# Kernel tuning notes

Hardware: AMD Instinct MI355X
Metric: run time of the kernel (lower is better)

The kernel has to match this reference:

```python
import jax, jax.numpy as jnp
import numpy as np

B, T, F, D, H, DFF, L = 8, 1024, 64, 512, 8, 2048, 3
DH = D // H
PERIODS = np.array([16, 256, 4096], np.int32)
CMS_LRS = np.array([0.01, 0.001, 0.0001], np.float32)
TITANS_LR = 0.01
TITANS_CLIP = 0.1


def layernorm(x, w, b):
    m = x.mean(-1, keepdims=True)
    v = x.var(-1, keepdims=True)
    return (x - m) * jax.lax.rsqrt(v + 1e-5) * w + b


def setup_inputs() -> dict:
    key = jax.random.key(0)
    ks = jax.random.split(key, 40)
    f32 = jnp.float32
    def rn(i, shape, s=0.02):
        return jax.random.normal(ks[i], shape, f32) * s
    inp = {
        'x': jax.random.normal(ks[0], (B, T, F), f32),
        'titans_W': jnp.zeros((D, D), f32),
        'cms_summary': jnp.zeros((L, D), f32),
        'cms_buf_sum': jnp.zeros((L, D), f32),
        'cms_count': jnp.zeros((L,), jnp.int32),
        'cms_step': jnp.zeros((L,), jnp.int32),
        'in_norm_w': jnp.ones((F,), f32), 'in_norm_b': jnp.zeros((F,), f32),
        'in_proj_W': rn(1, (D, F)), 'in_proj_b': jnp.zeros((D,), f32),
        'W_base': rn(2, (D, D), 0.01),
        'tit_out_W': rn(3, (D, D)), 'tit_out_b': jnp.zeros((D,), f32),
        'gate_W': rn(4, (L, D, D)), 'gate_b': jnp.zeros((L, D), f32),
        'comb_W': rn(5, (D, L * D)), 'comb_b': jnp.zeros((D,), f32),
        'n1_w': jnp.ones((D,), f32), 'n1_b': jnp.zeros((D,), f32),
        'qkv_W': rn(6, (3 * D, D)), 'qkv_b': jnp.zeros((3 * D,), f32),
        'ao_W': rn(7, (D, D)), 'ao_b': jnp.zeros((D,), f32),
        'n2_w': jnp.ones((D,), f32), 'n2_b': jnp.zeros((D,), f32),
        'f1_W': rn(8, (DFF, D)), 'f1_b': jnp.zeros((DFF,), f32),
        'f2_W': rn(9, (D, DFF)), 'f2_b': jnp.zeros((D,), f32),
        'fn_w': jnp.ones((D,), f32), 'fn_b': jnp.zeros((D,), f32),
        'head_W': rn(10, (1, D)), 'head_b': jnp.zeros((1,), f32),
    }
    return inp


def cms_tick_all(means, summary, buf_sum, count, step, gate_W, gate_b):
    """Sequential tick over T timesteps, vectorized over the L levels.
    means: [T, D] batch-mean of final hidden at each timestep."""
    periods = jnp.asarray(PERIODS)
    lrs = jnp.asarray(CMS_LRS)
    def step_fn(carry, m):
        summ, bs, cnt, stp = carry
        bs = bs + m[None, :]              # [L, D]
        cnt = cnt + 1
        stp = stp + 1
        fire = cnt >= periods              # [L]
        acc = bs / cnt.astype(bs.dtype)[:, None]
        g = jax.nn.sigmoid(jnp.einsum('lij,lj->li', gate_W, acc) + gate_b)
        new_summ = jnp.where(fire[:, None], (1.0 - lrs)[:, None] * summ + lrs[:, None] * g * acc, summ)
        bs = jnp.where(fire[:, None], jnp.zeros_like(bs), bs)
        cnt = jnp.where(fire, jnp.zeros_like(cnt), cnt)
        return (new_summ, bs, cnt, stp), None
    (summary, buf_sum, count, step), _ = jax.lax.scan(step_fn, (summary, buf_sum, count, step), means)
    return summary, buf_sum, count, step


def reference(x, titans_W, cms_summary, cms_buf_sum, cms_count, cms_step,
              in_norm_w, in_norm_b, in_proj_W, in_proj_b,
              W_base, tit_out_W, tit_out_b,
              gate_W, gate_b, comb_W, comb_b,
              n1_w, n1_b, qkv_W, qkv_b, ao_W, ao_b,
              n2_w, n2_b, f1_W, f1_b, f2_W, f2_b,
              fn_w, fn_b, head_W, head_b):
    # input norm + projection: [B,T,F] -> [B,T,D]
    h = layernorm(x, in_norm_w, in_norm_b) @ in_proj_W.T + in_proj_b
    # Titans fast-weight read
    W = W_base + titans_W
    tit = (h @ W.T) @ tit_out_W.T + tit_out_b
    # Titans fast-weight update (detached in the original)
    hs = jax.lax.stop_gradient(h)
    target = hs.mean(axis=1)               # [B, D]
    query = hs[:, -1, :]                   # [B, D]
    pred_m = query @ titans_W.T
    err = (target - pred_m).mean(axis=0)   # [D]
    grad = jnp.outer(err, query.mean(axis=0))
    gn = jnp.linalg.norm(grad)
    grad = jnp.where(gn > TITANS_CLIP, grad * (TITANS_CLIP / gn), grad)
    new_W = titans_W + TITANS_LR * grad
    h = h + tit
    # CMS residual from current summaries: concat [L*D] -> combine -> [D]
    cms_out = cms_summary.reshape(L * D) @ comb_W.T + comb_b
    h = h + cms_out                        # broadcast over [B,T,D]
    # transformer block (pre-norm, causal MHA)
    hn = layernorm(h, n1_w, n1_b)
    qkv = hn @ qkv_W.T + qkv_b
    q, k, v = jnp.split(qkv, 3, axis=-1)
    def to_heads(t):
        return t.reshape(B, T, H, DH).transpose(0, 2, 1, 3)
    q, k, v = to_heads(q), to_heads(k), to_heads(v)
    scores = jnp.einsum('bhqd,bhkd->bhqk', q, k) / np.sqrt(DH).astype(np.float32)
    causal = jnp.triu(jnp.ones((T, T), bool), 1)
    scores = jnp.where(causal, -jnp.inf, scores)
    attn = jax.nn.softmax(scores, axis=-1)
    ao = jnp.einsum('bhqk,bhkd->bhqd', attn, v).transpose(0, 2, 1, 3).reshape(B, T, D)
    h = h + ao @ ao_W.T + ao_b
    hn2 = layernorm(h, n2_w, n2_b)
    h = h + jax.nn.gelu(hn2 @ f1_W.T + f1_b, approximate=False) @ f2_W.T + f2_b
    h = layernorm(h, fn_w, fn_b)
    pred = (h @ head_W.T + head_b).squeeze(-1)   # [B, T]
    # CMS tick over all T steps (detached in the original)
    means = jax.lax.stop_gradient(h).mean(axis=0)  # [T, D]
    ns, nb, nc, nt = cms_tick_all(means, cms_summary, cms_buf_sum, cms_count, cms_step, gate_W, gate_b)
    return pred, new_W, ns, nb, nc, nt
```

## Files before the change

kernel.cpp:

```cpp
#include <hip/hip_runtime.h>
#include <hip/hip_bf16.h>
#include <math.h>

#define Bdim 8
#define Tdim 1024
#define Fdim 64
#define Ddim 512
#define Lcms 3

#define OFF_PRED 0
#define OFF_W    8192
#define OFF_NS   270336
#define OFF_NB   271872
#define OFF_NC   273408
#define OFF_NT   273411

typedef __hip_bfloat16 bf16;
typedef __attribute__((ext_vector_type(8))) short s8;
typedef __attribute__((ext_vector_type(4))) float f4;

__device__ __forceinline__ float b2f(bf16 v){ return __bfloat162float(v); }
__device__ __forceinline__ bf16  f2b(float v){ return __float2bfloat16(v); }
__device__ __forceinline__ short fb16(float v){ bf16 t = __float2bfloat16(v); return *reinterpret_cast<short*>(&t); }
__device__ __forceinline__ float toF(float v){ return v; }
__device__ __forceinline__ float toF(bf16 v){ return __bfloat162float(v); }
template<typename T> __device__ __forceinline__ T fromF(float v);
template<> __device__ __forceinline__ float fromF<float>(float v){ return v; }
template<> __device__ __forceinline__ bf16  fromF<bf16 >(float v){ return f2b(v); }

__device__ __forceinline__ f4 mfma16(s8 a, s8 b, f4 c){
  return __builtin_amdgcn_mfma_f32_16x16x32_bf16(a, b, c, 0, 0, 0);
}

__device__ __forceinline__ void gload16(const bf16* g, bf16* l){
  __builtin_amdgcn_global_load_lds(
      (const __attribute__((address_space(1))) unsigned*)g,
      (__attribute__((address_space(3))) unsigned*)l, 16, 0, 0);
}

__device__ __forceinline__ float gelu_fast(float x){
  float z2 = 1.5957691216f*(x + 0.044715f*x*x*x);
  z2 = fminf(fmaxf(z2, -18.f), 18.f);
  return x / (1.f + __expf(-z2));
}

__global__ __launch_bounds__(256) void k_conv_all(
    const void* s0, const void* s1, const void* s2, const void* s3,
    const void* s4, const void* s5, const void* s6, const void* s7,
    const void* s8v, const void* s9, const void* s10, const void* s11,
    const void* s12, const void* s13,
    bf16* __restrict__ dst, const unsigned* __restrict__ w1, int* __restrict__ flag,
    const int* __restrict__ cnt, int* __restrict__ params){
  bool isbf = (w1[0] == 0x3F803F80u);
  if (blockIdx.x==0 && threadIdx.x==0){
    flag[0] = isbf ? 1 : 0;
    const int P[3] = {16,256,4096};
    for (int l=0;l<3;l++){
      int c0 = cnt[l];
      int t1 = P[l] - c0 - 1; if (t1 < 0) t1 = 0;
      int K = (t1 >= Tdim) ? 0 : 1 + (Tdim-1-t1)/P[l];
      params[l*4+0]=t1; params[l*4+1]=K; params[l*4+2]=c0+t1+1; params[l*4+3]=c0;
    }
  }
  const void* srcs[14] = {s0,s1,s2,s3,s4,s5,s6,s7,s8v,s9,s10,s11,s12,s13};
  const int   ns[14]   = {262144,512,786432,1536,262144,512,1048576,2048,1048576,512,
                          32768,512,786432,1536};
  int gstride = gridDim.x*blockDim.x;
  int gid = blockIdx.x*blockDim.x + threadIdx.x;
  int base = 0;
  #pragma unroll
  for (int s=0;s<14;s++){
    int n = ns[s];
    if (isbf){
      const short* sp = (const short*)srcs[s]; short* dp = (short*)(dst+base);
      for (int i=gid;i<n;i+=gstride) dp[i] = sp[i];
    } else {
      const float* sp = (const float*)srcs[s];
      for (int i=gid;i<n;i+=gstride) dst[base+i] = f2b(sp[i]);
    }
    base += n;
  }
}

template<typename TW>
__device__ __forceinline__ void lnx_impl(const TW* x, const TW* nw, const TW* nb_, bf16* xn){
  int row = blockIdx.x*4 + (threadIdx.x>>6);
  int lane = threadIdx.x & 63;
  float v = toF(x[(size_t)row*Fdim + lane]);
  float s = v, s2 = v*v;
  #pragma unroll
  for (int off=32; off; off>>=1){ s += __shfl_down(s,off); s2 += __shfl_down(s2,off); }
  s = __shfl(s, 0); s2 = __shfl(s2, 0);
  float mu = s*(1.f/64.f);
  float var = s2*(1.f/64.f) - mu*mu;
  float rstd = rsqrtf(var + 1e-5f);
  xn[(size_t)row*Fdim + lane] = f2b((v-mu)*rstd*toF(nw[lane]) + toF(nb_[lane]));
}
__global__ __launch_bounds__(256) void k_lnx(const void* x, const void* nw, const void* nb_,
    bf16* xn, const int* flg){
  if (*flg) lnx_impl<bf16>((const bf16*)x,(const bf16*)nw,(const bf16*)nb_,xn);
  else      lnx_impl<float>((const float*)x,(const float*)nw,(const float*)nb_,xn);
}

__global__ __launch_bounds__(256) void k_reduce_tq1(const bf16* __restrict__ h,
    float* __restrict__ redtmp){
  int b = blockIdx.x>>5, chunk = blockIdx.x&31;
  int tid = threadIdx.x;
  #pragma unroll
  for (int o=0;o<2;o++){
    int d = tid + o*256;
    const bf16* p = h + ((size_t)b*Tdim + chunk*32)*Ddim + d;
    float s = 0.f;
    #pragma unroll
    for (int t=0;t<32;t++) s += b2f(p[(size_t)t*Ddim]);
    redtmp[((size_t)b*32 + chunk)*Ddim + d] = s;
  }
}

template<typename TW>
__device__ __forceinline__ void misc1_impl(const TW* Wbse, const TW* tW, bf16* Wout,
    const TW* summ, const TW* combW, const TW* combb, float* outv,
    const bf16* h, const float* redtmp, float* target, float* query){
  int blk = blockIdx.x, tid = threadIdx.x;
  if (blk < 1024){
    int i = blk*256 + tid;
    Wout[i] = f2b(toF(Wbse[i]) + toF(tW[i]));
  } else if (blk < 1152){
    __shared__ float s_s[Lcms*Ddim];
    for (int i=tid;i<Lcms*Ddim;i+=256) s_s[i] = toF(summ[i]);
    __syncthreads();
    int wave = tid>>6, lane = tid&63;
    int d = (blk-1024)*4 + wave;
    const TW* wr = combW + (size_t)d*(Lcms*Ddim);
    float a = 0.f;
    for (int j=lane;j<Lcms*Ddim;j+=64) a += s_s[j]*toF(wr[j]);
    #pragma unroll
    for (int off=32; off; off>>=1) a += __shfl_down(a,off);
    if (lane==0) outv[d] = a + toF(combb[d]);
  } else {
    int i = (blk-1152)*256 + tid;
    int b = i>>9, d = i&511;
    float s = 0.f;
    #pragma unroll
    for (int c=0;c<32;c++) s += redtmp[((size_t)b*32+c)*Ddim + d];
    target[i] = s*(1.f/(float)Tdim);
    query[i]  = b2f(h[((size_t)b*Tdim + (Tdim-1))*Ddim + d]);
  }
}
__global__ __launch_bounds__(256) void k_misc1(const void* Wbse, const void* tW, bf16* Wout,
    const void* summ, const void* combW, const void* combb, float* outv,
    const bf16* h, const float* redtmp, float* target, float* query, const int* flg){
  if (*flg) misc1_impl<bf16>((const bf16*)Wbse,(const bf16*)tW,Wout,(const bf16*)summ,
                             (const bf16*)combW,(const bf16*)combb,outv,h,redtmp,target,query);
  else      misc1_impl<float>((const float*)Wbse,(const float*)tW,Wout,(const float*)summ,
                             (const float*)combW,(const float*)combb,outv,h,redtmp,target,query);
}

template<typename TW>
__device__ __forceinline__ void titans_err_impl(const float* target, const float* query,
    const TW* tW, float* err, float* qmean){
  int wave = threadIdx.x>>6, lane = threadIdx.x&63;
  int d = blockIdx.x*4 + wave;
  const TW* wr = tW + (size_t)d*Ddim;
  float s = 0.f;
  #pragma unroll
  for (int b=0;b<Bdim;b++){
    const float* q = query + b*Ddim;
    float p = 0.f;
    for (int j=lane;j<Ddim;j+=64) p += q[j]*toF(wr[j]);
    s += p;
  }
  #pragma unroll
  for (int off=32; off; off>>=1) s += __shfl_down(s,off);
  if (lane==0){
    float e=0.f, qm=0.f;
    #pragma unroll
    for (int b=0;b<Bdim;b++){ e += target[b*Ddim+d]; qm += query[b*Ddim+d]; }
    err[d]   = (e - s)*(1.f/(float)Bdim);
    qmean[d] = qm*(1.f/(float)Bdim);
  }
}
__global__ __launch_bounds__(256) void k_titans_err(const float* target, const float* query,
    const void* tW, float* err, float* qmean, const int* flg){
  if (*flg) titans_err_impl<bf16>(target,query,(const bf16*)tW,err,qmean);
  else      titans_err_impl<float>(target,query,(const float*)tW,err,qmean);
}

template<typename TW>
__device__ __forceinline__ void new_W_impl(const TW* tW, const float* err, const float* qmean,
    TW* outW){
  int tid = threadIdx.x;
  float a = err[tid]*err[tid] + err[tid+256]*err[tid+256];
  float b = qmean[tid]*qmean[tid] + qmean[tid+256]*qmean[tid+256];
  #pragma unroll
  for (int off=32; off; off>>=1){ a += __shfl_down(a,off); b += __shfl_down(b,off); }
  __shared__ float sa[4], sb[4];
  int lane = tid & 63, wid = tid >> 6;
  if (lane==0){ sa[wid]=a; sb[wid]=b; }
  __syncthreads();
  float A = sa[0]+sa[1]+sa[2]+sa[3];
  float Bq= sb[0]+sb[1]+sb[2]+sb[3];
  float gn = sqrtf(A*Bq);
  float sf = 0.01f * (gn > 0.1f ? 0.1f/gn : 1.0f);
  int i = blockIdx.x*256 + tid;
  int r = i >> 9, c = i & 511;
  outW[i] = fromF<TW>(toF(tW[i]) + sf*err[r]*qmean[c]);
}
__global__ __launch_bounds__(256) void k_new_W(const void* tW, const float* err,
    const float* qmean, void* out, const int* flg){
  if (*flg) new_W_impl<bf16>((const bf16*)tW, err, qmean, ((bf16*)out)+OFF_W);
  else      new_W_impl<float>((const float*)tW, err, qmean, ((float*)out)+OFF_W);
}

template<int MODE, int DEPTH>
__global__ __launch_bounds__(512) void gemm_mfma(const bf16* __restrict__ A,
    const bf16* __restrict__ Bw, const bf16* __restrict__ bias,
    const float* __restrict__ colvec, bf16* __restrict__ Cout,
    const bf16* __restrict__ resid, int M, int N, int K){
  __shared__ __align__(16) bf16 As[DEPTH][128*32];
  __shared__ __align__(16) bf16 Bs[DEPTH][128*32];
  int tid = threadIdx.x, wave = tid>>6, lane = tid&63, quad = lane>>4, l16 = lane&15;
  int row0 = blockIdx.x*128, col0 = blockIdx.y*128;
  int wr = (wave>>2)*64, wc = (wave&3)*32;
  int srow = wave*16 + (lane>>2);
  int scol = (((lane&3) ^ ((lane>>3)&3)))*8;
  int rswz = (quad ^ ((l16>>1)&3))*8;
  f4 acc[8] = {};
  int niter = K >> 5;
  #define STAGE(bu, k0) { \
    gload16(A  + (size_t)(row0 + srow)*K + (k0) + scol, &As[bu][wave*512 + lane*8]); \
    gload16(Bw + (size_t)(col0 + srow)*K + (k0) + scol, &Bs[bu][wave*512 + lane*8]); \
  }
  STAGE(0, 0)
  if (DEPTH >= 3 && niter > 1) STAGE(1, 32)
  if (DEPTH >= 4 && niter > 2) STAGE(2, 64)
  for (int k=0; k<niter; k++){
    int bu = k & (DEPTH-1);
    if (DEPTH == 2){
      if (k+1 < niter){
        STAGE((k+1)&1, (k+1)<<5)
        asm volatile("s_waitcnt vmcnt(2)" ::: "memory");
      } else {
        asm volatile("s_waitcnt vmcnt(0)" ::: "memory");
      }
    } else {
      if (k+3 < niter){
        STAGE((k+3)&3, (k+3)<<5)
        asm volatile("s_waitcnt vmcnt(6)" ::: "memory");
      } else if (k+2 < niter){
        asm volatile("s_waitcnt vmcnt(4)" ::: "memory");
      } else if (k+1 < niter){
        asm volatile("s_waitcnt vmcnt(2)" ::: "memory");
      } else {
        asm volatile("s_waitcnt vmcnt(0)" ::: "memory");
      }
    }
    __builtin_amdgcn_s_barrier();
    s8 af[4], bfv[2];
    #pragma unroll
    for (int i=0;i<4;i++) af[i]  = *reinterpret_cast<const s8*>(&As[bu][(wr + i*16 + l16)*32 + rswz]);
    #pragma unroll
    for (int j=0;j<2;j++) bfv[j] = *reinterpret_cast<const s8*>(&Bs[bu][(wc + j*16 + l16)*32 + rswz]);
    #pragma unroll
    for (int i=0;i<4;i++)
      #pragma unroll
      for (int j=0;j<2;j++)
        acc[i*2+j] = mfma16(af[i], bfv[j], acc[i*2+j]);
    asm volatile("s_waitcnt lgkmcnt(0)" ::: "memory");
    __builtin_amdgcn_s_barrier();
  }
  #undef STAGE
  #pragma unroll
  for (int i=0;i<4;i++){
    #pragma unroll
    for (int j=0;j<2;j++){
      int n = col0 + wc + j*16 + l16;
      f4 a = acc[i*2+j];
      #pragma unroll
      for (int r=0;r<4;r++){
        int m = row0 + wr + i*16 + quad*4 + r;
        float v = a[r];
        if (MODE & 1) v += b2f(bias[n]);
        if (MODE & 8) v += colvec[n];
        if (MODE & 4) v = gelu_fast(v);
        if (MODE & 2) v += b2f(resid[(size_t)m*Ddim + n]);
        Cout[(size_t)m*N + n] = f2b(v);
      }
    }
  }
}

template<typename TW, int HEAD>
__device__ __forceinline__ void ln_impl(const bf16* in, const TW* w, const TW* b, bf16* outp,
    const TW* hw, const TW* hb, TW* pred){
  int row = blockIdx.x;
  const bf16* r = in + (size_t)row*Ddim;
  int tid = threadIdx.x;
  float v0 = b2f(r[tid]), v1 = b2f(r[tid + 256]);
  float s = v0+v1, s2 = v0*v0 + v1*v1;
  #pragma unroll
  for (int off=32; off; off>>=1){ s += __shfl_down(s,off); s2 += __shfl_down(s2,off); }
  __shared__ float sa[4], sb[4], sc[4];
  int lane = tid & 63, wid = tid >> 6;
  if (lane==0){ sa[wid]=s; sb[wid]=s2; }
  __syncthreads();
  float ts  = sa[0]+sa[1]+sa[2]+sa[3];
  float ts2 = sb[0]+sb[1]+sb[2]+sb[3];
  float mu = ts*(1.f/(float)Ddim);
  float var = ts2*(1.f/(float)Ddim) - mu*mu;
  float rstd = rsqrtf(var + 1e-5f);
  float o0 = (v0-mu)*rstd*toF(w[tid])     + toF(b[tid]);
  float o1 = (v1-mu)*rstd*toF(w[tid+256]) + toF(b[tid+256]);
  outp[(size_t)row*Ddim + tid]       = f2b(o0);
  outp[(size_t)row*Ddim + tid + 256] = f2b(o1);
  if (HEAD){
    float sp = o0*toF(hw[tid]) + o1*toF(hw[tid+256]);
    #pragma unroll
    for (int off=32; off; off>>=1) sp += __shfl_down(sp,off);
    if (lane==0) sc[wid] = sp;
    __syncthreads();
    if (tid==0) pred[row] = fromF<TW>(sc[0]+sc[1]+sc[2]+sc[3] + toF(hb[0]));
  }
}
template<int HEAD>
__global__ __launch_bounds__(256) void k_ln(const bf16* in, const void* w, const void* b,
    bf16* outp, const void* hw, const void* hb, void* out, const int* flg){
  if (*flg) ln_impl<bf16,HEAD>(in,(const bf16*)w,(const bf16*)b,outp,
                               (const bf16*)hw,(const bf16*)hb,((bf16*)out)+OFF_PRED);
  else      ln_impl<float,HEAD>(in,(const float*)w,(const float*)b,outp,
                               (const float*)hw,(const float*)hb,((float*)out)+OFF_PRED);
}

__global__ __launch_bounds__(256) void k_attn_mfma(const bf16* __restrict__ qkv,
                                                   bf16* __restrict__ ao){
  int blk = blockIdx.x;
  int bh = blk & 63;
  int qt = 15 - (blk >> 6);
  int head = bh & 7, b = bh >> 3;
  __shared__ __align__(16) bf16 Ks[2][64][72];
  __shared__ __align__(16) unsigned Vt4[2][64*36];
  __shared__ __align__(16) bf16 Ps[4][16][72];
  int tid = threadIdx.x, wave = tid>>6, lane = tid&63, quad = lane>>4, l16 = lane&15;
  int q0w = qt*64 + wave*16;
  const bf16* basep = qkv + (size_t)b*Tdim*1536 + head*64;
  s8 qf0 = *reinterpret_cast<const s8*>(basep + (size_t)(q0w+l16)*1536 + quad*8);
  s8 qf1 = *reinterpret_cast<const s8*>(basep + (size_t)(q0w+l16)*1536 + 32 + quad*8);
  f4 o[4] = {{0,0,0,0},{0,0,0,0},{0,0,0,0},{0,0,0,0}};
  float m_r[4] = {-3.0e38f,-3.0e38f,-3.0e38f,-3.0e38f};
  float l_r[4] = {0.f,0.f,0.f,0.f};
  int key_s = tid>>3, dgk = (tid&7)*8;
  int vp = tid>>3, dgv = (tid&7)*8;
  int vu4 = (((vp>>2) ^ (tid&7)) & 7)*4 + (vp&3);
  int nch = qt + 1;
  s8 kr0[2], kr1[2], vra[2], vrb[2];
  {
    const bf16* kp = basep + (size_t)key_s*1536 + 512 + dgk;
    kr0[0] = *reinterpret_cast<const s8*>(kp);
    kr1[0] = *reinterpret_cast<const s8*>(kp + (size_t)32*1536);
    const bf16* vpa = basep + (size_t)(2*vp)*1536 + 1024 + dgv;
    vra[0] = *reinterpret_cast<const s8*>(vpa);
    vrb[0] = *reinterpret_cast<const s8*>(vpa + 1536);
    if (1 < nch){
      const bf16* kp1 = basep + (size_t)(64+key_s)*1536 + 512 + dgk;
      kr0[1] = *reinterpret_cast<const s8*>(kp1);
      kr1[1] = *reinterpret_cast<const s8*>(kp1 + (size_t)32*1536);
      const bf16* vpa1 = basep + (size_t)(64 + 2*vp)*1536 + 1024 + dgv;
      vra[1] = *reinterpret_cast<const s8*>(vpa1);
      vrb[1] = *reinterpret_cast<const s8*>(vpa1 + 1536);
    }
  }
  auto do_chunk = [&](int ch, int bu){
    f4 sc4[4] = {{0,0,0,0},{0,0,0,0},{0,0,0,0},{0,0,0,0}};
    #pragma unroll
    for (int t=0;t<4;t++){
      sc4[t] = mfma16(qf0, *reinterpret_cast<const s8*>(&Ks[bu][t*16+l16][quad*8]),    sc4[t]);
      sc4[t] = mfma16(qf1, *reinterpret_cast<const s8*>(&Ks[bu][t*16+l16][32+quad*8]), sc4[t]);
    }
    int key0 = ch*64 + l16;
    #pragma unroll
    for (int r=0;r<4;r++){
      int qrow = q0w + quad*4 + r;
      float a0 = (key0      <= qrow) ? sc4[0][r]*0.125f : -3.0e38f;
      float a1 = (key0 + 16 <= qrow) ? sc4[1][r]*0.125f : -3.0e38f;
      float a2 = (key0 + 32 <= qrow) ? sc4[2][r]*0.125f : -3.0e38f;
      float a3 = (key0 + 48 <= qrow) ? sc4[3][r]*0.125f : -3.0e38f;
      float mx = fmaxf(fmaxf(a0,a1), fmaxf(a2,a3));
      mx = fmaxf(mx, __shfl_xor(mx,1)); mx = fmaxf(mx, __shfl_xor(mx,2));
      mx = fmaxf(mx, __shfl_xor(mx,4)); mx = fmaxf(mx, __shfl_xor(mx,8));
      float mnew = fmaxf(m_r[r], mx);
      float al = __expf(m_r[r]-mnew); m_r[r] = mnew;
      float p0 = __expf(a0-mnew), p1 = __expf(a1-mnew);
      float p2 = __expf(a2-mnew), p3 = __expf(a3-mnew);
      float rs = (p0+p1)+(p2+p3);
      rs += __shfl_xor(rs,1); rs += __shfl_xor(rs,2);
      rs += __shfl_xor(rs,4); rs += __shfl_xor(rs,8);
      l_r[r] = l_r[r]*al + rs;
      o[0][r]*=al; o[1][r]*=al; o[2][r]*=al; o[3][r]*=al;
      int prow = quad*4+r;
      *reinterpret_cast<short*>(&Ps[wave][prow][l16])    = fb16(p0);
      *reinterpret_cast<short*>(&Ps[wave][prow][16+l16]) = fb16(p1);
      *reinterpret_cast<short*>(&Ps[wave][prow][32+l16]) = fb16(p2);
      *reinterpret_cast<short*>(&Ps[wave][prow][48+l16]) = fb16(p3);
    }
    asm volatile("s_waitcnt lgkmcnt(0)" ::: "memory");
    s8 pf0 = *reinterpret_cast<const s8*>(&Ps[wave][l16][quad*8]);
    s8 pf1 = *reinterpret_cast<const s8*>(&Ps[wave][l16][32+quad*8]);
    #pragma unroll
    for (int j=0;j<4;j++){
      int d = j*16 + l16;
      int swz = (d>>3) & 7;
      s8 b0 = *reinterpret_cast<const s8*>(&Vt4[bu][d*36 + ((quad   ^ swz))*4]);
      s8 b1 = *reinterpret_cast<const s8*>(&Vt4[bu][d*36 + (((4+quad)^ swz))*4]);
      o[j] = mfma16(pf0, b0, o[j]);
      o[j] = mfma16(pf1, b1, o[j]);
    }
  };
  for (int ch0=0; ch0<nch; ch0+=2){
    #pragma unroll
    for (int s=0;s<2;s++){
      if (ch0+s < nch){
        *reinterpret_cast<s8*>(&Ks[s][key_s][dgk])    = kr0[s];
        *reinterpret_cast<s8*>(&Ks[s][32+key_s][dgk]) = kr1[s];
        #pragma unroll
        for (int j=0;j<8;j++){
          unsigned w = (unsigned)(unsigned short)vra[s][j] | ((unsigned)(unsigned short)vrb[s][j] << 16);
          Vt4[s][(dgv+j)*36 + vu4] = w;
        }
      }
    }
    __syncthreads();
    #pragma unroll
    for (int s=0;s<2;s++){
      int chn = ch0 + 2 + s;
      if (chn < nch){
        const bf16* kp = basep + (size_t)(chn*64+key_s)*1536 + 512 + dgk;
        kr0[s] = *reinterpret_cast<const s8*>(kp);
        kr1[s] = *reinterpret_cast<const s8*>(kp + (size_t)32*1536);
        const bf16* vpa = basep + (size_t)(chn*64 + 2*vp)*1536 + 1024 + dgv;
        vra[s] = *reinterpret_cast<const s8*>(vpa);
        vrb[s] = *reinterpret_cast<const s8*>(vpa + 1536);
      }
    }
    do_chunk(ch0, 0);
    if (ch0+1 < nch) do_chunk(ch0+1, 1);
    if (ch0+2 < nch) __syncthreads();
  }
  #pragma unroll
  for (int r=0;r<4;r++){
    float inv = 1.f/l_r[r];
    size_t rowb = (size_t)(b*Tdim + q0w + quad*4 + r)*Ddim + head*64;
    ao[rowb + l16]      = f2b(o[0][r]*inv);
    ao[rowb + 16 + l16] = f2b(o[1][r]*inv);
    ao[rowb + 32 + l16] = f2b(o[2][r]*inv);
    ao[rowb + 48 + l16] = f2b(o[3][r]*inv);
  }
}

__global__ void k_means(const bf16* __restrict__ h, float* __restrict__ means){
  int i = blockIdx.x*256 + threadIdx.x;
  float s = 0.f;
  #pragma unroll
  for (int b=0;b<Bdim;b++) s += b2f(h[(size_t)b*Tdim*Ddim + i]);
  means[i] = s*(1.f/(float)Bdim);
}

template<typename TW>
__device__ __forceinline__ void cms_acc_impl(const float* means, const TW* bs0,
    const int* params, float* acc, bf16* acch, float* tailtmp){
  int tid = threadIdx.x;
  if (blockIdx.x < 384){
    int l = blockIdx.x>>7, k = blockIdx.x&127;
    int K = params[l*4+1];
    if (k >= K){
      for (int d=tid; d<Ddim; d+=256) acch[((size_t)l*128+k)*Ddim + d] = f2b(0.f);
      return;
    }
    int t1 = params[l*4], cnt0 = params[l*4+2];
    const int P[3] = {16,256,4096};
    int lo = (k==0) ? 0 : t1 + (k-1)*P[l] + 1;
    int hi = t1 + k*P[l];
    float inv = 1.f/((k==0) ? (float)cnt0 : (float)P[l]);
    int lane = tid&63, strip = tid>>6;
    __shared__ float red[4][Ddim];
    float4 a0 = {0,0,0,0}, a1 = {0,0,0,0};
    for (int t=lo+strip; t<=hi; t+=4){
      const float4* row = (const float4*)(means + (size_t)t*Ddim);
      float4 v0 = row[lane], v1 = row[lane+64];
      a0.x+=v0.x; a0.y+=v0.y; a0.z+=v0.z; a0.w+=v0.w;
      a1.x+=v1.x; a1.y+=v1.y; a1.z+=v1.z; a1.w+=v1.w;
    }
    ((float4*)red[strip])[lane]    = a0;
    ((float4*)red[strip])[lane+64] = a1;
    __syncthreads();
    for (int d=tid; d<Ddim; d+=256){
      float s = red[0][d]+red[1][d]+red[2][d]+red[3][d];
      if (k==0) s += toF(bs0[l*Ddim+d]);
      float v = s*inv;
      acc[((size_t)l*65+k)*Ddim + d] = v;
      acch[((size_t)l*128+k)*Ddim + d] = f2b(v);
    }
  } else {
    int bb = blockIdx.x - 384;
    int l = bb>>5, chunk = bb&31;
    int t1 = params[l*4], K = params[l*4+1];
    const int P[3] = {16,256,4096};
    int lo = (K==0) ? 0 : t1 + (K-1)*P[l] + 1;
    int f = tid & 127, strip = tid >> 7;
    int tbeg = chunk*32, tend = tbeg + 32;
    if (tbeg < lo) tbeg = lo;
    float4 a = {0,0,0,0};
    for (int t=tbeg+strip; t<tend; t+=2){
      float4 v = ((const float4*)(means + (size_t)t*Ddim))[f];
      a.x+=v.x; a.y+=v.y; a.z+=v.z; a.w+=v.w;
    }
    __shared__ float4 redt[2][128];
    redt[strip][f] = a;
    __syncthreads();
    if (strip==0){
      float4 b = redt[1][f];
      a.x+=b.x; a.y+=b.y; a.z+=b.z; a.w+=b.w;
      ((float4*)(tailtmp + ((size_t)l*32 + chunk)*Ddim))[f] = a;
    }
  }
}
__global__ __launch_bounds__(256) void k_cms_acc(const float* means, const void* bs0,
    const int* params, float* acc, bf16* acch, float* tailtmp, const int* flg){
  if (*flg) cms_acc_impl<bf16>(means,(const bf16*)bs0,params,acc,acch,tailtmp);
  else      cms_acc_impl<float>(means,(const float*)bs0,params,acc,acch,tailtmp);
}

__global__ __launch_bounds__(256) void k_cms_gate_mfma(const bf16* __restrict__ accbh,
    const bf16* __restrict__ wg, const bf16* __restrict__ wgb, float* __restrict__ g){
  int l = blockIdx.y;
  const bf16* A  = accbh + (size_t)l*128*Ddim;
  const bf16* Bw = wg    + (size_t)l*Ddim*Ddim;
  __shared__ __align__(16) bf16 As[128*32];
  __shared__ __align__(16) bf16 Bs[128*32];
  int tid = threadIdx.x, wave = tid>>6, lane = tid&63, quad = lane>>4, l16 = lane&15;
  int col0 = blockIdx.x*128;
  int wr = (wave>>1)*64, wc = (wave&1)*64;
  int srow = lane>>2, scol = (lane&3)*8;
  f4 acc[16] = {};
  for (int k0=0; k0<Ddim; k0+=32){
    __syncthreads();
    #pragma unroll
    for (int it=0; it<2; it++){
      int c = wave*2 + it;
      gload16(A  + (size_t)(c*16 + srow)*Ddim + k0 + scol, &As[c*512 + lane*8]);
      gload16(Bw + (size_t)(col0 + c*16 + srow)*Ddim + k0 + scol, &Bs[c*512 + lane*8]);
    }
    __syncthreads();
    s8 af[4], bfv[4];
    #pragma unroll
    for (int i=0;i<4;i++) af[i]  = *reinterpret_cast<const s8*>(&As[(wr + i*16 + l16)*32 + quad*8]);
    #pragma unroll
    for (int j=0;j<4;j++) bfv[j] = *reinterpret_cast<const s8*>(&Bs[(wc + j*16 + l16)*32 + quad*8]);
    #pragma unroll
    for (int i=0;i<4;i++)
      #pragma unroll
      for (int j=0;j<4;j++)
        acc[i*4+j] = mfma16(af[i], bfv[j], acc[i*4+j]);
  }
  #pragma unroll
  for (int i=0;i<4;i++){
    #pragma unroll
    for (int j=0;j<4;j++){
      int n = col0 + wc + j*16 + l16;
      f4 a = acc[i*4+j];
      #pragma unroll
      for (int r=0;r<4;r++){
        int m = wr + i*16 + quad*4 + r;
        if (m < 65){
          float v = a[r] + b2f(wgb[l*Ddim + n]);
          g[((size_t)l*65 + m)*Ddim + n] = 1.f/(1.f + __expf(-v));
        }
      }
    }
  }
}

template<typename TW>
__device__ __forceinline__ void cms_final_impl(const float* acc, const float* g,
    const float* tailtmp, const TW* summ0, const TW* bs0, const int* params,
    const int* step0, TW* out){
  int l = blockIdx.x;
  int t1 = params[l*4], K = params[l*4+1], c0 = params[l*4+3];
  const int P[3] = {16,256,4096};
  const float LR[3] = {0.01f,0.001f,0.0001f};
  float lr = LR[l];
  for (int d=threadIdx.x; d<Ddim; d+=256){
    float s = toF(summ0[l*Ddim + d]);
    for (int k=0;k<K;k++)
      s = (1.f-lr)*s + lr*g[((size_t)l*65+k)*Ddim+d]*acc[((size_t)l*65+k)*Ddim+d];
    out[OFF_NS + l*Ddim + d] = fromF<TW>(s);
    float nbv = (K==0) ? toF(bs0[l*Ddim+d]) : 0.f;
    #pragma unroll
    for (int c=0;c<32;c++) nbv += tailtmp[((size_t)l*32+c)*Ddim + d];
    out[OFF_NB + l*Ddim + d] = fromF<TW>(nbv);
  }
  if (threadIdx.x==0){
    int nc = (K==0) ? c0 + Tdim : (Tdim-1 - (t1 + (K-1)*P[l]));
    out[OFF_NC + l] = fromF<TW>((float)nc);
    out[OFF_NT + l] = fromF<TW>((float)(step0[l] + Tdim));
  }
}
__global__ __launch_bounds__(256) void k_cms_final(const float* acc, const float* g,
    const float* tailtmp, const void* summ0, const void* bs0, const int* params,
    const int* step0, void* out, const int* flg){
  if (*flg) cms_final_impl<bf16>(acc,g,tailtmp,(const bf16*)summ0,(const bf16*)bs0,params,step0,(bf16*)out);
  else      cms_final_impl<float>(acc,g,tailtmp,(const float*)summ0,(const float*)bs0,params,step0,(float*)out);
}

extern "C" void kernel_launch(void* const* d_in, const int* in_sizes, int n_in,
                              void* d_out, int out_size, void* d_ws, size_t ws_size,
                              hipStream_t stream) {
  (void)in_sizes; (void)n_in; (void)out_size; (void)ws_size;
  const void* x           = d_in[0];
  const void* titansW     = d_in[1];
  const void* cms_summary = d_in[2];
  const void* cms_bufsum  = d_in[3];
  const int*  cms_count   = (const int*)d_in[4];
  const int*  cms_step    = (const int*)d_in[5];
  const void* in_norm_w   = d_in[6];
  const void* in_norm_b   = d_in[7];
  const void* in_proj_W   = d_in[8];
  const void* in_proj_b   = d_in[9];
  const void* W_base      = d_in[10];
  const void* tit_out_W   = d_in[11];
  const void* tit_out_b   = d_in[12];
  const void* gate_W      = d_in[13];
  const void* gate_b      = d_in[14];
  const void* comb_W      = d_in[15];
  const void* comb_b      = d_in[16];
  const void* n1_w        = d_in[17];
  const void* n1_b        = d_in[18];
  const void* qkv_W       = d_in[19];
  const void* qkv_b       = d_in[20];
  const void* ao_W        = d_in[21];
  const void* ao_b        = d_in[22];
  const void* n2_w        = d_in[23];
  const void* n2_b        = d_in[24];
  const void* f1_W        = d_in[25];
  const void* f1_b        = d_in[26];
  const void* f2_W        = d_in[27];
  const void* f2_b        = d_in[28];
  const void* fn_w        = d_in[29];
  const void* fn_b        = d_in[30];
  const void* head_W      = d_in[31];
  const void* head_b      = d_in[32];

  char* u8 = (char*)d_ws;
  bf16*  h     = (bf16*)(u8 + 0);
  bf16*  hnA   = (bf16*)(u8 + 8388608);
  bf16*  big   = (bf16*)(u8 + 16777216);
  bf16*  xn    = big;
  bf16*  tmid  = big + (size_t)8192*1536;
  float* means = (float*)(u8 + 50331648);
  bf16*  Wb    = (bf16*)(u8 + 52428800);
  bf16*  wall  = (bf16*)(u8 + 52953088);
  bf16*  wtit  = wall;
  bf16*  wtitb = wall + 262144;
  bf16*  wqkv  = wall + 262656;
  bf16*  wqkvb = wall + 1049088;
  bf16*  wao   = wall + 1050624;
  bf16*  waob  = wall + 1312768;
  bf16*  wf1   = wall + 1313280;
  bf16*  wf1b  = wall + 2361856;
  bf16*  wf2   = wall + 2363904;
  bf16*  wf2b  = wall + 3412480;
  bf16*  wproj = wall + 3412992;
  bf16*  wprojb= wall + 3445760;
  bf16*  wgate = wall + 3446272;
  bf16*  wgateb= wall + 4232704;
  float* target= (float*)(u8 + 61421568);
  float* query = (float*)(u8 + 61437952);
  float* errv  = (float*)(u8 + 61454336);
  float* qmean = (float*)(u8 + 61456384);
  float* cmsout= (float*)(u8 + 61458944);
  float* accb  = (float*)(u8 + 61460992);
  float* gbuf  = (float*)(u8 + 61860352);
  bf16*  accbh = (bf16*) (u8 + 62259712);
  int*   params= (int*)  (u8 + 62652928);
  int*   dflag = (int*)  (u8 + 62652992);
  float* redtmp= (float*)(u8 + 62659584);
  float* tailtmp=(float*)(u8 + 63183872);

  k_conv_all<<<1024, 256, 0, stream>>>(tit_out_W, tit_out_b, qkv_W, qkv_b, ao_W, ao_b,
                                       f1_W, f1_b, f2_W, f2_b, in_proj_W, in_proj_b,
                                       gate_W, gate_b, wall, (const unsigned*)in_norm_w,
                                       dflag, cms_count, params);
  k_lnx<<<2048, 256, 0, stream>>>(x, in_norm_w, in_norm_b, xn, dflag);
  gemm_mfma<1,2><<<dim3(64,4), 512, 0, stream>>>(xn, wproj, wprojb, nullptr, h, nullptr, 8192, 512, 64);
  k_reduce_tq1<<<256, 256, 0, stream>>>(h, redtmp);
  k_misc1<<<1168, 256, 0, stream>>>(W_base, titansW, Wb, cms_summary, comb_W, comb_b,
                                    cmsout, h, redtmp, target, query, dflag);
  k_titans_err<<<128, 256, 0, stream>>>(target, query, titansW, errv, qmean, dflag);
  k_new_W<<<1024, 256, 0, stream>>>(titansW, errv, qmean, d_out, dflag);
  gemm_mfma<0,4><<<dim3(64,4), 512, 0, stream>>>(h, Wb, nullptr, nullptr, tmid, nullptr, 8192, 512, 512);
  gemm_mfma<11,4><<<dim3(64,4), 512, 0, stream>>>(tmid, wtit, wtitb, cmsout, h, h, 8192, 512, 512);
  k_ln<0><<<8192, 256, 0, stream>>>(h, n1_w, n1_b, hnA, nullptr, nullptr, nullptr, dflag);
  gemm_mfma<1,2><<<dim3(64,12), 512, 0, stream>>>(hnA, wqkv, wqkvb, nullptr, big, nullptr, 8192, 1536, 512);
  k_attn_mfma<<<1024, 256, 0, stream>>>(big, tmid);
  gemm_mfma<3,4><<<dim3(64,4), 512, 0, stream>>>(tmid, wao, waob, nullptr, h, h, 8192, 512, 512);
  k_ln<0><<<8192, 256, 0, stream>>>(h, n2_w, n2_b, hnA, nullptr, nullptr, nullptr, dflag);
  gemm_mfma<5,2><<<dim3(64,16), 512, 0, stream>>>(hnA, wf1, wf1b, nullptr, big, nullptr, 8192, 2048, 512);
  gemm_mfma<3,4><<<dim3(64,4), 512, 0, stream>>>(big, wf2, wf2b, nullptr, h, h, 8192, 512, 2048);
  k_ln<1><<<8192, 256, 0, stream>>>(h, fn_w, fn_b, hnA, head_W, head_b, d_out, dflag);
  k_means<<<2048, 256, 0, stream>>>(hnA, means);
  k_cms_acc<<<480, 256, 0, stream>>>(means, cms_bufsum, params, accb, accbh, tailtmp, dflag);
  k_cms_gate_mfma<<<dim3(4,3), 256, 0, stream>>>(accbh, wgate, wgateb, gbuf);
  k_cms_final<<<Lcms, 256, 0, stream>>>(accb, gbuf, tailtmp, cms_summary, cms_bufsum, params, cms_step, d_out, dflag);
}
```

Baseline: 442.8 us.

## Merge front-end prep kernels and fuse final layernorm with head and batch means

Folds weight conversion, input layernorm, W_base+titans_W sum and the CMS combine matvec into one k_front launch. The leftover target/query reduction moves to a small k_tq2 kernel. The final layernorm is now one block per timestep covering all 8 batch rows with vectorized 16-byte loads, computing the head prediction and the batch means in the same pass. This drops the separate k_means pass over the hidden state and cuts launch count, at the cost of a larger mixed-role kernel and fewer blocks (1024) for the final LN.

```diff
diff --git a/kernel.cpp b/kernel.cpp
--- a/kernel.cpp
+++ b/kernel.cpp
@@ -22,6 +22,7 @@
 __device__ __forceinline__ float b2f(bf16 v){ return __bfloat162float(v); }
 __device__ __forceinline__ bf16  f2b(float v){ return __float2bfloat16(v); }
 __device__ __forceinline__ short fb16(float v){ bf16 t = __float2bfloat16(v); return *reinterpret_cast<short*>(&t); }
+__device__ __forceinline__ float sh2f(short s){ bf16 t = *reinterpret_cast<bf16*>(&s); return __bfloat162float(t); }
 __device__ __forceinline__ float toF(float v){ return v; }
 __device__ __forceinline__ float toF(bf16 v){ return __bfloat162float(v); }
 template<typename T> __device__ __forceinline__ T fromF(float v);
@@ -44,15 +45,53 @@
   return x / (1.f + __expf(-z2));
 }
 
-__global__ __launch_bounds__(256) void k_conv_all(
+template<typename TW>
+__device__ __forceinline__ void front_misc(int blk, int tid,
+    const TW* x, const TW* nw, const TW* nb_, bf16* xn,
+    const TW* Wbse, const TW* tW, bf16* Wout,
+    const TW* summ, const TW* combW, const TW* combb, float* outv){
+  if (blk < 2048){
+    int row = blk*4 + (tid>>6);
+    int lane = tid & 63;
+    float v = toF(x[(size_t)row*Fdim + lane]);
+    float s = v, s2 = v*v;
+    #pragma unroll
+    for (int off=32; off; off>>=1){ s += __shfl_down(s,off); s2 += __shfl_down(s2,off); }
+    s = __shfl(s, 0); s2 = __shfl(s2, 0);
+    float mu = s*(1.f/64.f);
+    float var = s2*(1.f/64.f) - mu*mu;
+    float rstd = rsqrtf(var + 1e-5f);
+    xn[(size_t)row*Fdim + lane] = f2b((v-mu)*rstd*toF(nw[lane]) + toF(nb_[lane]));
+  } else if (blk < 3072){
+    int i = (blk-2048)*256 + tid;
+    Wout[i] = f2b(toF(Wbse[i]) + toF(tW[i]));
+  } else {
+    __shared__ float s_s[Lcms*Ddim];
+    for (int i=tid;i<Lcms*Ddim;i+=256) s_s[i] = toF(summ[i]);
+    __syncthreads();
+    int wave = tid>>6, lane = tid&63;
+    int d = (blk-3072)*4 + wave;
+    const TW* wr = combW + (size_t)d*(Lcms*Ddim);
+    float a = 0.f;
+    for (int j=lane;j<Lcms*Ddim;j+=64) a += s_s[j]*toF(wr[j]);
+    #pragma unroll
+    for (int off=32; off; off>>=1) a += __shfl_down(a,off);
+    if (lane==0) outv[d] = a + toF(combb[d]);
+  }
+}
+__global__ __launch_bounds__(256) void k_front(
     const void* s0, const void* s1, const void* s2, const void* s3,
     const void* s4, const void* s5, const void* s6, const void* s7,
     const void* s8v, const void* s9, const void* s10, const void* s11,
     const void* s12, const void* s13,
     bf16* __restrict__ dst, const unsigned* __restrict__ w1, int* __restrict__ flag,
-    const int* __restrict__ cnt, int* __restrict__ params){
+    const int* __restrict__ cnt, int* __restrict__ params,
+    const void* x, const void* nw, const void* nb_, bf16* xn,
+    const void* Wbse, const void* tW, bf16* Wout,
+    const void* summ, const void* combW, const void* combb, float* outv){
   bool isbf = (w1[0] == 0x3F803F80u);
-  if (blockIdx.x==0 && threadIdx.x==0){
+  int blk = blockIdx.x, tid = threadIdx.x;
+  if (blk==0 && tid==0){
     flag[0] = isbf ? 1 : 0;
     const int P[3] = {16,256,4096};
     for (int l=0;l<3;l++){
@@ -62,44 +101,34 @@
       params[l*4+0]=t1; params[l*4+1]=K; params[l*4+2]=c0+t1+1; params[l*4+3]=c0;
     }
   }
-  const void* srcs[14] = {s0,s1,s2,s3,s4,s5,s6,s7,s8v,s9,s10,s11,s12,s13};
-  const int   ns[14]   = {262144,512,786432,1536,262144,512,1048576,2048,1048576,512,
-                          32768,512,786432,1536};
-  int gstride = gridDim.x*blockDim.x;
-  int gid = blockIdx.x*blockDim.x + threadIdx.x;
-  int base = 0;
-  #pragma unroll
-  for (int s=0;s<14;s++){
-    int n = ns[s];
-    if (isbf){
-      const short* sp = (const short*)srcs[s]; short* dp = (short*)(dst+base);
-      for (int i=gid;i<n;i+=gstride) dp[i] = sp[i];
-    } else {
-      const float* sp = (const float*)srcs[s];
-      for (int i=gid;i<n;i+=gstride) dst[base+i] = f2b(sp[i]);
-    }
-    base += n;
-  }
-}
-
-template<typename TW>
-__device__ __forceinline__ void lnx_impl(const TW* x, const TW* nw, const TW* nb_, bf16* xn){
-  int row = blockIdx.x*4 + (threadIdx.x>>6);
-  int lane = threadIdx.x & 63;
-  float v = toF(x[(size_t)row*Fdim + lane]);
-  float s = v, s2 = v*v;
-  #pragma unroll
-  for (int off=32; off; off>>=1){ s += __shfl_down(s,off); s2 += __shfl_down(s2,off); }
-  s = __shfl(s, 0); s2 = __shfl(s2, 0);
-  float mu = s*(1.f/64.f);
-  float var = s2*(1.f/64.f) - mu*mu;
-  float rstd = rsqrtf(var + 1e-5f);
-  xn[(size_t)row*Fdim + lane] = f2b((v-mu)*rstd*toF(nw[lane]) + toF(nb_[lane]));
-}
-__global__ __launch_bounds__(256) void k_lnx(const void* x, const void* nw, const void* nb_,
-    bf16* xn, const int* flg){
-  if (*flg) lnx_impl<bf16>((const bf16*)x,(const bf16*)nw,(const bf16*)nb_,xn);
-  else      lnx_impl<float>((const float*)x,(const float*)nw,(const float*)nb_,xn);
+  if (blk < 1024){
+    const void* srcs[14] = {s0,s1,s2,s3,s4,s5,s6,s7,s8v,s9,s10,s11,s12,s13};
+    const int   ns[14]   = {262144,512,786432,1536,262144,512,1048576,2048,1048576,512,
+                            32768,512,786432,1536};
+    const int gstride = 1024*256;
+    int gid = blk*256 + tid;
+    int base = 0;
+    #pragma unroll
+    for (int s=0;s<14;s++){
+      int n = ns[s];
+      if (isbf){
+        const short* sp = (const short*)srcs[s]; short* dp = (short*)(dst+base);
+        for (int i=gid;i<n;i+=gstride) dp[i] = sp[i];
+      } else {
+        const float* sp = (const float*)srcs[s];
+        for (int i=gid;i<n;i+=gstride) dst[base+i] = f2b(sp[i]);
+      }
+      base += n;
+    }
+  } else {
+    int b2 = blk - 1024;
+    if (isbf) front_misc<bf16>(b2, tid, (const bf16*)x,(const bf16*)nw,(const bf16*)nb_,xn,
+                               (const bf16*)Wbse,(const bf16*)tW,Wout,
+                               (const bf16*)summ,(const bf16*)combW,(const bf16*)combb,outv);
+    else      front_misc<float>(b2, tid, (const float*)x,(const float*)nw,(const float*)nb_,xn,
+                               (const float*)Wbse,(const float*)tW,Wout,
+                               (const float*)summ,(const float*)combW,(const float*)combb,outv);
+  }
 }
 
 __global__ __launch_bounds__(256) void k_reduce_tq1(const bf16* __restrict__ h,
@@ -116,44 +145,15 @@
     redtmp[((size_t)b*32 + chunk)*Ddim + d] = s;
   }
 }
-
-template<typename TW>
-__device__ __forceinline__ void misc1_impl(const TW* Wbse, const TW* tW, bf16* Wout,
-    const TW* summ, const TW* combW, const TW* combb, float* outv,
-    const bf16* h, const float* redtmp, float* target, float* query){
-  int blk = blockIdx.x, tid = threadIdx.x;
-  if (blk < 1024){
-    int i = blk*256 + tid;
-    Wout[i] = f2b(toF(Wbse[i]) + toF(tW[i]));
-  } else if (blk < 1152){
-    __shared__ float s_s[Lcms*Ddim];
-    for (int i=tid;i<Lcms*Ddim;i+=256) s_s[i] = toF(summ[i]);
-    __syncthreads();
-    int wave = tid>>6, lane = tid&63;
-    int d = (blk-1024)*4 + wave;
-    const TW* wr = combW + (size_t)d*(Lcms*Ddim);
-    float a = 0.f;
-    for (int j=lane;j<Lcms*Ddim;j+=64) a += s_s[j]*toF(wr[j]);
-    #pragma unroll
-    for (int off=32; off; off>>=1) a += __shfl_down(a,off);
-    if (lane==0) outv[d] = a + toF(combb[d]);
-  } else {
-    int i = (blk-1152)*256 + tid;
-    int b = i>>9, d = i&511;
-    float s = 0.f;
-    #pragma unroll
-    for (int c=0;c<32;c++) s += redtmp[((size_t)b*32+c)*Ddim + d];
-    target[i] = s*(1.f/(float)Tdim);
-    query[i]  = b2f(h[((size_t)b*Tdim + (Tdim-1))*Ddim + d]);
-  }
-}
-__global__ __launch_bounds__(256) void k_misc1(const void* Wbse, const void* tW, bf16* Wout,
-    const void* summ, const void* combW, const void* combb, float* outv,
-    const bf16* h, const float* redtmp, float* target, float* query, const int* flg){
-  if (*flg) misc1_impl<bf16>((const bf16*)Wbse,(const bf16*)tW,Wout,(const bf16*)summ,
-                             (const bf16*)combW,(const bf16*)combb,outv,h,redtmp,target,query);
-  else      misc1_impl<float>((const float*)Wbse,(const float*)tW,Wout,(const float*)summ,
-                             (const float*)combW,(const float*)combb,outv,h,redtmp,target,query);
+__global__ void k_tq2(const bf16* __restrict__ h, const float* __restrict__ redtmp,
+    float* __restrict__ target, float* __restrict__ query){
+  int i = blockIdx.x*256 + threadIdx.x;
+  int b = i>>9, d = i&511;
+  float s = 0.f;
+  #pragma unroll
+  for (int c=0;c<32;c++) s += redtmp[((size_t)b*32+c)*Ddim + d];
+  target[i] = s*(1.f/(float)Tdim);
+  query[i]  = b2f(h[((size_t)b*Tdim + (Tdim-1))*Ddim + d]);
 }
 
 template<typename TW>
@@ -290,9 +290,8 @@
   }
 }
 
-template<typename TW, int HEAD>
-__device__ __forceinline__ void ln_impl(const bf16* in, const TW* w, const TW* b, bf16* outp,
-    const TW* hw, const TW* hb, TW* pred){
+template<typename TW>
+__device__ __forceinline__ void ln_impl(const bf16* in, const TW* w, const TW* b, bf16* outp){
   int row = blockIdx.x;
   const bf16* r = in + (size_t)row*Ddim;
   int tid = threadIdx.x;
@@ -300,7 +299,7 @@
   float s = v0+v1, s2 = v0*v0 + v1*v1;
   #pragma unroll
   for (int off=32; off; off>>=1){ s += __shfl_down(s,off); s2 += __shfl_down(s2,off); }
-  __shared__ float sa[4], sb[4], sc[4];
+  __shared__ float sa[4], sb[4];
   int lane = tid & 63, wid = tid >> 6;
   if (lane==0){ sa[wid]=s; sb[wid]=s2; }
   __syncthreads();
@@ -309,26 +308,68 @@
   float mu = ts*(1.f/(float)Ddim);
   float var = ts2*(1.f/(float)Ddim) - mu*mu;
   float rstd = rsqrtf(var + 1e-5f);
-  float o0 = (v0-mu)*rstd*toF(w[tid])     + toF(b[tid]);
-  float o1 = (v1-mu)*rstd*toF(w[tid+256]) + toF(b[tid+256]);
-  outp[(size_t)row*Ddim + tid]       = f2b(o0);
-  outp[(size_t)row*Ddim + tid + 256] = f2b(o1);
-  if (HEAD){
-    float sp = o0*toF(hw[tid]) + o1*toF(hw[tid+256]);
+  outp[(size_t)row*Ddim + tid]       = f2b((v0-mu)*rstd*toF(w[tid])     + toF(b[tid]));
+  outp[(size_t)row*Ddim + tid + 256] = f2b((v1-mu)*rstd*toF(w[tid+256]) + toF(b[tid+256]));
+}
+__global__ __launch_bounds__(256) void k_ln(const bf16* in, const void* w, const void* b,
+    bf16* outp, const int* flg){
+  if (*flg) ln_impl<bf16>(in,(const bf16*)w,(const bf16*)b,outp);
+  else      ln_impl<float>(in,(const float*)w,(const float*)b,outp);
+}
+
+template<typename TW>
+__device__ __forceinline__ void ln_hm_impl(const bf16* in, const TW* w, const TW* b,
+    bf16* outp, const TW* hw, const TW* hb, TW* pred, float* means){
+  int t = blockIdx.x;
+  int tid = threadIdx.x, wave = tid>>6, lane = tid&63;
+  int d0 = lane*8;
+  __shared__ float msum[4][Ddim];
+  float wv[8], bv[8], hwv[8];
+  #pragma unroll
+  for (int j=0;j<8;j++){ wv[j]=toF(w[d0+j]); bv[j]=toF(b[d0+j]); hwv[j]=toF(hw[d0+j]); }
+  float hb0 = toF(hb[0]);
+  float osum[8] = {0,0,0,0,0,0,0,0};
+  #pragma unroll
+  for (int rr=0; rr<2; rr++){
+    int bb = wave*2 + rr;
+    size_t row = (size_t)bb*Tdim + t;
+    s8 raw = *reinterpret_cast<const s8*>(in + row*Ddim + d0);
+    float v[8];
+    float s=0.f, s2=0.f;
+    #pragma unroll
+    for (int j=0;j<8;j++){ v[j]=sh2f(raw[j]); s+=v[j]; s2+=v[j]*v[j]; }
+    #pragma unroll
+    for (int off=32; off; off>>=1){ s += __shfl_down(s,off); s2 += __shfl_down(s2,off); }
+    s = __shfl(s,0); s2 = __shfl(s2,0);
+    float mu = s*(1.f/(float)Ddim);
+    float var = s2*(1.f/(float)Ddim) - mu*mu;
+    float rstd = rsqrtf(var + 1e-5f);
+    float sp = 0.f;
+    s8 ob;
+    #pragma unroll
+    for (int j=0;j<8;j++){
+      float o = (v[j]-mu)*rstd*wv[j] + bv[j];
+      ob[j] = fb16(o);
+      sp += o*hwv[j];
+      osum[j] += o;
+    }
+    *reinterpret_cast<s8*>(outp + row*Ddim + d0) = ob;
     #pragma unroll
     for (int off=32; off; off>>=1) sp += __shfl_down(sp,off);
-    if (lane==0) sc[wid] = sp;
-    __syncthreads();
-    if (tid==0) pred[row] = fromF<TW>(sc[0]+sc[1]+sc[2]+sc[3] + toF(hb[0]));
-  }
-}
-template<int HEAD>
-__global__ __launch_bounds__(256) void k_ln(const bf16* in, const void* w, const void* b,
-    bf16* outp, const void* hw, const void* hb, void* out, const int* flg){
-  if (*flg) ln_impl<bf16,HEAD>(in,(const bf16*)w,(const bf16*)b,outp,
-                               (const bf16*)hw,(const bf16*)hb,((bf16*)out)+OFF_PRED);
-  else      ln_impl<float,HEAD>(in,(const float*)w,(const float*)b,outp,
-                               (const float*)hw,(const float*)hb,((float*)out)+OFF_PRED);
+    if (lane==0) pred[row] = fromF<TW>(sp + hb0);
+  }
+  #pragma unroll
+  for (int j=0;j<8;j++) msum[wave][d0+j] = osum[j];
+  __syncthreads();
+  for (int d=tid; d<Ddim; d+=256)
+    means[(size_t)t*Ddim + d] = (msum[0][d]+msum[1][d]+msum[2][d]+msum[3][d])*(1.f/8.f);
+}
+__global__ __launch_bounds__(256) void k_ln_hm(const bf16* in, const void* w, const void* b,
+    bf16* outp, const void* hw, const void* hb, void* out, float* means, const int* flg){
+  if (*flg) ln_hm_impl<bf16>(in,(const bf16*)w,(const bf16*)b,outp,
+                             (const bf16*)hw,(const bf16*)hb,((bf16*)out)+OFF_PRED,means);
+  else      ln_hm_impl<float>(in,(const float*)w,(const float*)b,outp,
+                             (const float*)hw,(const float*)hb,((float*)out)+OFF_PRED,means);
 }
 
 __global__ __launch_bounds__(256) void k_attn_mfma(const bf16* __restrict__ qkv,
@@ -454,14 +495,6 @@
     ao[rowb + 32 + l16] = f2b(o[2][r]*inv);
     ao[rowb + 48 + l16] = f2b(o[3][r]*inv);
   }
-}
-
-__global__ void k_means(const bf16* __restrict__ h, float* __restrict__ means){
-  int i = blockIdx.x*256 + threadIdx.x;
-  float s = 0.f;
-  #pragma unroll
-  for (int b=0;b<Bdim;b++) s += b2f(h[(size_t)b*Tdim*Ddim + i]);
-  means[i] = s*(1.f/(float)Bdim);
 }
 
 template<typename TW>
@@ -685,28 +718,28 @@
   float* redtmp= (float*)(u8 + 62659584);
   float* tailtmp=(float*)(u8 + 63183872);
 
-  k_conv_all<<<1024, 256, 0, stream>>>(tit_out_W, tit_out_b, qkv_W, qkv_b, ao_W, ao_b,
-                                       f1_W, f1_b, f2_W, f2_b, in_proj_W, in_proj_b,
-                                       gate_W, gate_b, wall, (const unsigned*)in_norm_w,
-                                       dflag, cms_count, params);
-  k_lnx<<<2048, 256, 0, stream>>>(x, in_norm_w, in_norm_b, xn, dflag);
+  k_front<<<4224, 256, 0, stream>>>(tit_out_W, tit_out_b, qkv_W, qkv_b, ao_W, ao_b,
+                                    f1_W, f1_b, f2_W, f2_b, in_proj_W, in_proj_b,
+                                    gate_W, gate_b, wall, (const unsigned*)in_norm_w,
+                                    dflag, cms_count, params,
+                                    x, in_norm_w, in_norm_b, xn,
+                                    W_base, titansW, Wb,
+                                    cms_summary, comb_W, comb_b, cmsout);
   gemm_mfma<1,2><<<dim3(64,4), 512, 0, stream>>>(xn, wproj, wprojb, nullptr, h, nullptr, 8192, 512, 64);
   k_reduce_tq1<<<256, 256, 0, stream>>>(h, redtmp);
-  k_misc1<<<1168, 256, 0, stream>>>(W_base, titansW, Wb, cms_summary, comb_W, comb_b,
-                                    cmsout, h, redtmp, target, query, dflag);
+  k_tq2<<<16, 256, 0, stream>>>(h, redtmp, target, query);
   k_titans_err<<<128, 256, 0, stream>>>(target, query, titansW, errv, qmean, dflag);
   k_new_W<<<1024, 256, 0, stream>>>(titansW, errv, qmean, d_out, dflag);
   gemm_mfma<0,4><<<dim3(64,4), 512, 0, stream>>>(h, Wb, nullptr, nullptr, tmid, nullptr, 8192, 512, 512);
   gemm_mfma<11,4><<<dim3(64,4), 512, 0, stream>>>(tmid, wtit, wtitb, cmsout, h, h, 8192, 512, 512);
-  k_ln<0><<<8192, 256, 0, stream>>>(h, n1_w, n1_b, hnA, nullptr, nullptr, nullptr, dflag);
+  k_ln<<<8192, 256, 0, stream>>>(h, n1_w, n1_b, hnA, dflag);
   gemm_mfma<1,2><<<dim3(64,12), 512, 0, stream>>>(hnA, wqkv, wqkvb, nullptr, big, nullptr, 8192, 1536, 512);
   k_attn_mfma<<<1024, 256, 0, stream>>>(big, tmid);
   gemm_mfma<3,4><<<dim3(64,4), 512, 0, stream>>>(tmid, wao, waob, nullptr, h, h, 8192, 512, 512);
-  k_ln<0><<<8192, 256, 0, stream>>>(h, n2_w, n2_b, hnA, nullptr, nullptr, nullptr, dflag);
+  k_ln<<<8192, 256, 0, stream>>>(h, n2_w, n2_b, hnA, dflag);
   gemm_mfma<5,2><<<dim3(64,16), 512, 0, stream>>>(hnA, wf1, wf1b, nullptr, big, nullptr, 8192, 2048, 512);
   gemm_mfma<3,4><<<dim3(64,4), 512, 0, stream>>>(big, wf2, wf2b, nullptr, h, h, 8192, 512, 2048);
-  k_ln<1><<<8192, 256, 0, stream>>>(h, fn_w, fn_b, hnA, head_W, head_b, d_out, dflag);
-  k_means<<<2048, 256, 0, stream>>>(hnA, means);
+  k_ln_hm<<<1024, 256, 0, stream>>>(h, fn_w, fn_b, hnA, head_W, head_b, d_out, means, dflag);
   k_cms_acc<<<480, 256, 0, stream>>>(means, cms_bufsum, params, accb, accbh, tailtmp, dflag);
   k_cms_gate_mfma<<<dim3(4,3), 256, 0, stream>>>(accbh, wgate, wgateb, gbuf);
   k_cms_final<<<Lcms, 256, 0, stream>>>(accb, gbuf, tailtmp, cms_summary, cms_bufsum, params, cms_step, d_out, dflag);
```

Measured after the change: 435.1 us. No clear change (-1.7%).
